# Performance work log

Hardware: AMD Instinct MI355X
Metric: run time of the kernel (lower is better)

## Reference

```python
import jax, jax.numpy as jnp
import numpy as np

N = 262144          # batch size
C = 100             # num_classes
R0, R1 = 0.95, 1.0  # recall_range
LAM = 0.5           # lambda_pauc
LS = 0.1            # label_smoothing
MAX_PAUC = R1 - R0


def setup_inputs() -> dict:
    key = jax.random.key(0)
    k1, k2 = jax.random.split(key)
    predictions = jax.random.normal(k1, (N, C), dtype=jnp.float32)
    targets = jax.random.randint(k2, (N,), 0, C)
    weight = jnp.ones((C,), dtype=jnp.float32)
    return {"predictions": predictions, "targets": targets, "weight": weight}


def _roc_curves(scores, labels):
    """Vectorized per-class ROC. scores, labels: [C, N].
    Replaces the O(N^2) per-threshold loop with sort + cumsum (tie-correct:
    tp at threshold s_j counts ALL samples with score >= s_j)."""
    order = jnp.argsort(-scores, axis=1)                      # descending
    ss = jnp.take_along_axis(scores, order, axis=1)           # [C, N]
    sl = jnp.take_along_axis(labels, order, axis=1)           # [C, N]
    cpos = jnp.cumsum(sl, axis=1)                             # cumulative positives
    # last index within each tie-group of equal scores
    neg = -ss  # ascending
    idx = jax.vmap(lambda a: jnp.searchsorted(a, a, side='right'))(neg) - 1
    tp = jnp.take_along_axis(cpos, idx, axis=1)
    cnt = (idx + 1).astype(scores.dtype)
    fp = cnt - tp
    P = cpos[:, -1:]                       # total positives per class
    Nn = scores.shape[1] - P               # total negatives per class
    tpr = jnp.where(P > 0, tp / jnp.maximum(P, 1.0), 0.0)
    fpr = jnp.where(Nn > 0, fp / jnp.maximum(Nn, 1.0), 0.0)
    return fpr, tpr


def reference(predictions, targets, weight):
    probs = jax.nn.softmax(predictions, axis=1)               # [N, C]
    onehot = jnp.eye(C, dtype=predictions.dtype)[targets]     # [N, C]
    onehot_s = (1.0 - LS) * onehot + LS / C

    # per-class binary labels (smoothed true-class value > 0.5)
    labels = (onehot_s > 0.5).astype(predictions.dtype).T     # [C, N]
    scores = probs.T                                          # [C, N]

    fpr, tpr = _roc_curves(scores, labels)
    mask = (tpr >= R0) & (tpr <= R1)
    y = jnp.maximum(tpr - R0, 0.0)
    # tpr is monotone non-decreasing, so the recall mask is contiguous and
    # trapz over the masked subset == sum over adjacent pairs both in mask.
    pm = (mask[:, :-1] & mask[:, 1:]).astype(predictions.dtype)
    pauc = jnp.sum(0.5 * (y[:, :-1] + y[:, 1:]) * (fpr[:, 1:] - fpr[:, :-1]) * pm, axis=1)  # [C]

    avg_p_auc = jnp.sum(pauc * weight) / (jnp.sum(weight) * MAX_PAUC)
    # torch computes TP/FP via .item(): the pAUC path carries no gradient
    avg_p_auc = jax.lax.stop_gradient(jnp.clip(avg_p_auc, 0.0, 1.0))

    log_probs = jax.nn.log_softmax(predictions, axis=1)
    ce_loss = -jnp.mean(jnp.sum(onehot_s * log_probs * weight, axis=1))
    pauc_loss = 1.0 - avg_p_auc ** 2
    return (1.0 - LAM) * ce_loss + LAM * pauc_loss
```

## Files before the change

kernel.cpp:

```cpp
#include <hip/hip_runtime.h>
#include <math.h>

#define WAVE 64
constexpr int   CC      = 100;
constexpr int   MAXM    = 160;
constexpr int   BUCKET  = 4096;
constexpr int   USTRIDE = 161;
constexpr int   LCAP    = 4096;
constexpr float LSMOOTH = 0.1f;
constexpr int   TILE    = 64;
constexpr int   K3AGRID = 1024;
constexpr int   K3BGRID = 512;

__global__ __launch_bounds__(256) void k1_tile(
    const float* __restrict__ pred, const int* __restrict__ targets,
    const float* __restrict__ weight, float* __restrict__ L_out,
    float* __restrict__ pos_out, float* __restrict__ ce_partial, int N)
{
    __shared__ float tile[TILE * CC];
    __shared__ int   ttgt[TILE];
    __shared__ float tL[TILE], tpos[TILE];
    __shared__ float cered[4];
    const int tid = threadIdx.x;
    const int r0  = blockIdx.x * TILE;

    const float4* src = (const float4*)(pred + (size_t)r0 * CC);
    #pragma unroll
    for (int t = tid; t < TILE * (CC / 4); t += 256)
        *((float4*)&tile[t * 4]) = src[t];
    if (tid < TILE) ttgt[tid] = targets[r0 + tid];
    __syncthreads();

    const int x = tid & 15;
    const int G = tid >> 4;
    float w[7];
    #pragma unroll
    for (int j = 0; j < 7; ++j) {
        int c = x + 16 * j;
        w[j] = (c < CC) ? weight[c] : 0.0f;
    }
    float Wl = 0.0f;
    #pragma unroll
    for (int j = 0; j < 7; ++j) Wl += w[j];
    #pragma unroll
    for (int off = 1; off < 16; off <<= 1) Wl += __shfl_xor(Wl, off, 16);

    float ce_acc = 0.0f;
    #pragma unroll
    for (int rr = 0; rr < 4; ++rr) {
        const int r = G * 4 + rr;
        const float* rp = tile + r * CC;
        float v[7];
        #pragma unroll
        for (int j = 0; j < 7; ++j) {
            int c = x + 16 * j;
            v[j] = (c < CC) ? rp[c] : -INFINITY;
        }
        float vmax = v[0];
        #pragma unroll
        for (int j = 1; j < 7; ++j) vmax = fmaxf(vmax, v[j]);
        #pragma unroll
        for (int off = 1; off < 16; off <<= 1) vmax = fmaxf(vmax, __shfl_xor(vmax, off, 16));
        float z = 0.0f, ws = 0.0f;
        #pragma unroll
        for (int j = 0; j < 7; ++j) {
            int c = x + 16 * j;
            if (c < CC) { z += __expf(v[j] - vmax); ws += w[j] * v[j]; }
        }
        #pragma unroll
        for (int off = 1; off < 16; off <<= 1) {
            z  += __shfl_xor(z,  off, 16);
            ws += __shfl_xor(ws, off, 16);
        }
        float L = vmax + __logf(z);
        if (x == 0) {
            int t = ttgt[r];
            float pt = rp[t];
            tL[r] = L; tpos[r] = pt - L;
            ce_acc += -((1.0f - LSMOOTH) * weight[t] * (pt - L)
                        + (LSMOOTH / CC) * (ws - Wl * L));
        }
    }
    #pragma unroll
    for (int off = 32; off; off >>= 1) ce_acc += __shfl_xor(ce_acc, off, WAVE);
    if ((tid & 63) == 0) cered[tid >> 6] = ce_acc;
    __syncthreads();
    if (tid < TILE) {
        L_out[r0 + tid]   = tL[tid];
        pos_out[r0 + tid] = tpos[tid];
    }
    if (tid == 0)
        ce_partial[blockIdx.x] = cered[0] + cered[1] + cered[2] + cered[3];
}

__global__ __launch_bounds__(256) void k1b_scatter(
    const int* __restrict__ targets, const float* __restrict__ pos,
    int* __restrict__ cls_cnt, float* __restrict__ bucket, int N)
{
    __shared__ int hist[CC];
    __shared__ int base[CC];
    __shared__ int loc[CC];
    const int tid = threadIdx.x;
    const int rowsPerBlock = N / gridDim.x;
    const int r0 = blockIdx.x * rowsPerBlock;
    const int r1 = r0 + rowsPerBlock;
    for (int c = tid; c < CC; c += blockDim.x) { hist[c] = 0; loc[c] = 0; }
    __syncthreads();
    for (int r = r0 + tid; r < r1; r += blockDim.x)
        atomicAdd(&hist[targets[r]], 1);
    __syncthreads();
    for (int c = tid; c < CC; c += blockDim.x)
        base[c] = (hist[c] > 0) ? atomicAdd(&cls_cnt[c], hist[c]) : 0;
    __syncthreads();
    for (int r = r0 + tid; r < r1; r += blockDim.x) {
        int c = targets[r];
        int idx = base[c] + atomicAdd(&loc[c], 1);
        if (idx < BUCKET) bucket[(size_t)c * BUCKET + idx] = pos[r];
    }
}

__global__ __launch_bounds__(256) void k2_select(
    const float* __restrict__ bucket, const int* __restrict__ cls_cnt,
    float* __restrict__ u, int* __restrict__ m_arr, int* __restrict__ P_arr,
    float* __restrict__ wm_arr)
{
    __shared__ unsigned int keys[BUCKET];
    __shared__ unsigned int hist[256];
    __shared__ unsigned int scan[256];
    __shared__ unsigned int sel[256];
    __shared__ unsigned int s_prefix;
    __shared__ int s_rank;
    __shared__ int cnt_lt;
    const int c   = blockIdx.x;
    const int tid = threadIdx.x;
    const int P = min(cls_cnt[c], BUCKET);
    double Kd = 0.95 * (double)P;
    int kf = (int)floor(Kd);
    int m = P - kf;
    if (m > MAXM) m = MAXM;
    if (m < 0) m = 0;
    if (tid == 0) {
        m_arr[c] = m; P_arr[c] = P;
        wm_arr[c] = (float)((double)(kf + 1) - Kd);
        s_prefix = 0; s_rank = m - 1; cnt_lt = 0;
    }
    for (int i = tid; i < P; i += 256) {
        unsigned int b = __float_as_uint(bucket[(size_t)c * BUCKET + i]);
        keys[i] = (b & 0x80000000u) ? ~b : (b | 0x80000000u);
    }
    __syncthreads();
    if (m == 0) return;

    for (int shift = 24; shift >= 0; shift -= 8) {
        hist[tid] = 0;
        __syncthreads();
        unsigned int pref = s_prefix;
        for (int i = tid; i < P; i += 256) {
            unsigned int k = keys[i];
            bool match = (shift == 24) || ((k >> (shift + 8)) == pref);
            if (match) atomicAdd(&hist[(k >> shift) & 255u], 1u);
        }
        __syncthreads();
        if (tid < 64) {
            unsigned h0 = hist[tid*4], h1 = hist[tid*4+1],
                     h2 = hist[tid*4+2], h3 = hist[tid*4+3];
            unsigned s0 = h0, s1 = s0 + h1, s2 = s1 + h2, s3 = s2 + h3;
            unsigned sc = s3;
            #pragma unroll
            for (int off = 1; off < 64; off <<= 1) {
                unsigned t2 = __shfl_up(sc, (unsigned)off, 64);
                if (tid >= off) sc += t2;
            }
            unsigned excl = sc - s3;
            scan[tid*4]   = excl + s0;
            scan[tid*4+1] = excl + s1;
            scan[tid*4+2] = excl + s2;
            scan[tid*4+3] = excl + s3;
        }
        __syncthreads();
        int r = s_rank;
        unsigned int inc = scan[tid];
        unsigned int exc = inc - hist[tid];
        __syncthreads();
        if ((unsigned int)r >= exc && (unsigned int)r < inc) {
            s_rank   = r - (int)exc;
            s_prefix = (pref << 8) | (unsigned int)tid;
        }
        __syncthreads();
    }
    const unsigned int kth = s_prefix;

    for (int i = tid; i < P; i += 256) {
        unsigned int k = keys[i];
        if (k < kth) {
            int pslot = atomicAdd(&cnt_lt, 1);
            sel[pslot] = k;
        }
    }
    __syncthreads();
    const int nlt = cnt_lt;
    for (int j = nlt + tid; j < 256; j += 256) sel[j] = (j < m) ? kth : 0xFFFFFFFFu;
    __syncthreads();
    for (int kk = 2; kk <= 256; kk <<= 1) {
        for (int j = kk >> 1; j > 0; j >>= 1) {
            int i = tid, ixj = tid ^ j;
            if (ixj > i) {
                unsigned int a = sel[i], b = sel[ixj];
                bool up = ((i & kk) == 0);
                if ((a > b) == up) { sel[i] = b; sel[ixj] = a; }
            }
            __syncthreads();
        }
    }
    if (tid < m) {
        unsigned int k = sel[tid];
        unsigned int b = (k & 0x80000000u) ? (k & 0x7fffffffu) : ~k;
        u[c * MAXM + tid] = __uint_as_float(b);
    }
}

__device__ __forceinline__ int ubound(const float* uc, int m, float key, int maxidx) {
    int l = 0;
    #pragma unroll
    for (int s = 128; s; s >>= 1) {
        int p = l + s - 1;
        float val = uc[p < maxidx ? p : maxidx];
        l += ((p < m) && (val <= key)) ? s : 0;
    }
    return l;
}

__global__ __launch_bounds__(256) void k3a_stream(
    const float4* __restrict__ pred4, const float* __restrict__ L,
    const float* __restrict__ u, const int* __restrict__ m_arr,
    uint2* __restrict__ list, int* __restrict__ list_cnt, int list_cap,
    int* __restrict__ g_cnt, int* __restrict__ g_sum, int total4)
{
    __shared__ float umax_s[CC];
    __shared__ uint2 buf[LCAP];
    __shared__ int lcnt;
    __shared__ int gbase;
    const int tid  = threadIdx.x;
    const int lane = tid & 63;
    if (tid < CC) {
        int m = m_arr[tid];
        umax_s[tid] = (m > 0) ? u[tid * MAXM + m - 1] : -INFINITY;
    }
    if (tid == 0) lcnt = 0;
    __syncthreads();

    auto pushq = [&](bool qual, int c, float sc) {
        unsigned long long mask = __ballot(qual);
        if (mask == 0ull) return;
        int lead = __ffsll((long long)mask) - 1;
        int nq   = __popcll(mask);
        int base = 0;
        if (lane == lead) base = atomicAdd(&lcnt, nq);
        base = __shfl(base, lead);
        if (qual) {
            int my  = __popcll(mask & ((1ull << lane) - 1ull));
            int idx = base + my;
            if (idx < LCAP) {
                buf[idx] = make_uint2((unsigned int)c, __float_as_uint(sc));
            } else {
                int m = m_arr[c];
                int l = ubound(u + c * MAXM, m, sc, MAXM - 1);
                atomicAdd(&g_cnt[c], 1);
                atomicAdd(&g_sum[c], m - 1 - l);
            }
        }
    };

    auto proc = [&](float4 v, float Ln, int j) {
        float4 um = *((const float4*)&umax_s[j * 4]);
        pushq(v.x - Ln < um.x, j * 4 + 0, v.x - Ln);
        pushq(v.y - Ln < um.y, j * 4 + 1, v.y - Ln);
        pushq(v.z - Ln < um.z, j * 4 + 2, v.z - Ln);
        pushq(v.w - Ln < um.w, j * 4 + 3, v.w - Ln);
    };

    const int stride = K3AGRID * 256;
    int i = blockIdx.x * 256 + tid;
    while (i < total4) {
        const int ia = i + stride, ib = i + 2 * stride, ic = i + 3 * stride;
        const bool ha = ia < total4, hb = ib < total4, hc = ic < total4;
        float4 v0 = pred4[i];
        float4 va = ha ? pred4[ia] : make_float4(0.f, 0.f, 0.f, 0.f);
        float4 vb = hb ? pred4[ib] : make_float4(0.f, 0.f, 0.f, 0.f);
        float4 vc = hc ? pred4[ic] : make_float4(0.f, 0.f, 0.f, 0.f);
        int n0 = i / 25, j0 = i - n0 * 25;
        float L0 = L[n0];
        proc(v0, L0, j0);
        if (ha) { int na = ia / 25, ja = ia - na * 25; proc(va, L[na], ja); }
        if (hb) { int nb = ib / 25, jb = ib - nb * 25; proc(vb, L[nb], jb); }
        if (hc) { int nc = ic / 25, jc = ic - nc * 25; proc(vc, L[nc], jc); }
        i += 4 * stride;
    }
    __syncthreads();
    int cnt = min(lcnt, LCAP);
    if (tid == 0) gbase = atomicAdd(list_cnt, cnt);
    __syncthreads();
    const int base0 = gbase;
    for (int k = tid; k < cnt; k += 256) {
        int gi = base0 + k;
        if (gi < list_cap) {
            list[gi] = buf[k];
        } else {
            uint2 e = buf[k];
            int c = (int)e.x; float sc = __uint_as_float(e.y);
            int m = m_arr[c];
            int l = ubound(u + c * MAXM, m, sc, MAXM - 1);
            atomicAdd(&g_cnt[c], 1);
            atomicAdd(&g_sum[c], m - 1 - l);
        }
    }
}

__global__ __launch_bounds__(256) void k3b_rank_final(
    const uint2* __restrict__ list, const int* __restrict__ list_cnt, int list_cap,
    const float* __restrict__ u, const int* __restrict__ m_arr,
    const int* __restrict__ P_arr, const float* __restrict__ wm_arr,
    const float* __restrict__ weight, const float* __restrict__ ce_partial,
    int nPartial, int* __restrict__ g_cnt, int* __restrict__ g_sum,
    int* __restrict__ done, float* __restrict__ out, int N)
{
    __shared__ float us[CC * USTRIDE];
    __shared__ int sm[CC], lcnt[CC], lsum[CC];
    __shared__ int lastflag;
    __shared__ double r1[256], r2[256], r3[256];
    const int tid = threadIdx.x;
    for (int c = tid; c < CC; c += 256) { sm[c] = m_arr[c]; lcnt[c] = 0; lsum[c] = 0; }
    for (int t = tid; t < CC * MAXM; t += 256) {
        int c = t / MAXM, k = t - c * MAXM;
        us[c * USTRIDE + k] = u[t];
    }
    __syncthreads();
    const int n = min(*list_cnt, list_cap);
    const int stride = K3BGRID * 256;
    for (int base = blockIdx.x * 256 + tid; base < n; base += 4 * stride) {
        int  cc4[4]; int mm4[4]; float kk4[4]; bool hh4[4];
        #pragma unroll
        for (int t = 0; t < 4; ++t) {
            int idx = base + t * stride;
            bool h = idx < n;
            uint2 e = h ? list[idx] : make_uint2(0u, 0u);
            hh4[t] = h;
            cc4[t] = (int)e.x;
            mm4[t] = h ? sm[(int)e.x] : 0;
            kk4[t] = __uint_as_float(e.y);
        }
        int ll4[4] = {0, 0, 0, 0};
        #pragma unroll
        for (int s = 128; s; s >>= 1) {
            #pragma unroll
            for (int t = 0; t < 4; ++t) {
                int p = ll4[t] + s - 1;
                float val = us[cc4[t] * USTRIDE + (p < USTRIDE - 1 ? p : USTRIDE - 1)];
                ll4[t] += ((p < mm4[t]) && (val <= kk4[t])) ? s : 0;
            }
        }
        #pragma unroll
        for (int t = 0; t < 4; ++t)
            if (hh4[t]) {
                atomicAdd(&lcnt[cc4[t]], 1);
                atomicAdd(&lsum[cc4[t]], mm4[t] - 1 - ll4[t]);
            }
    }
    __syncthreads();
    for (int c = tid; c < CC; c += 256)
        if (lcnt[c]) { atomicAdd(&g_cnt[c], lcnt[c]); atomicAdd(&g_sum[c], lsum[c]); }
    __threadfence();
    __syncthreads();
    if (tid == 0) {
        int r = atomicAdd(done, 1);
        lastflag = (r == (int)gridDim.x - 1) ? 1 : 0;
    }
    __syncthreads();
    if (!lastflag) return;

    double ce = 0.0;
    for (int t = tid; t < nPartial; t += 256) ce += (double)ce_partial[t];
    double p = 0.0, wsum = 0.0;
    for (int c = tid; c < CC; c += 256) {
        int P = P_arr[c], m = m_arr[c];
        double wgt = (double)weight[c];
        long long Nn = (long long)N - P;
        if (P > 0 && Nn > 0 && m > 0) {
            int gc = __hip_atomic_load(&g_cnt[c], __ATOMIC_RELAXED, __HIP_MEMORY_SCOPE_AGENT);
            int gs = __hip_atomic_load(&g_sum[c], __ATOMIC_RELAXED, __HIP_MEMORY_SCOPE_AGENT);
            double wm = (double)wm_arr[c];
            double S   = (double)gs + wm * (double)gc;
            double sub = 0.5 * (double)(m - 1) * (double)(m - 2) + wm * (double)(m - 1);
            double pc  = (S - sub) / ((double)Nn * (double)P);
            if (pc < 0.0) pc = 0.0;
            p += pc * wgt;
        }
        wsum += wgt;
    }
    r1[tid] = ce; r2[tid] = p; r3[tid] = wsum;
    __syncthreads();
    for (int off = 128; off; off >>= 1) {
        if (tid < off) {
            r1[tid] += r1[tid + off];
            r2[tid] += r2[tid + off];
            r3[tid] += r3[tid + off];
        }
        __syncthreads();
    }
    if (tid == 0) {
        double ce_loss = r1[0] / (double)N;
        double avg = r2[0] / (r3[0] * 0.05);
        avg = fmin(fmax(avg, 0.0), 1.0);
        out[0] = (float)(0.5 * ce_loss + 0.5 * (1.0 - avg * avg));
    }
}

extern "C" void kernel_launch(void* const* d_in, const int* in_sizes, int n_in,
                              void* d_out, int out_size, void* d_ws, size_t ws_size,
                              hipStream_t stream) {
    (void)n_in; (void)out_size;
    const float* pred    = (const float*)d_in[0];
    const int*   targets = (const int*)d_in[1];
    const float* weight  = (const float*)d_in[2];
    float* out = (float*)d_out;
    const int N = in_sizes[1];

    const int K1_BLOCKS = N / TILE;
    char* base = (char*)d_ws;
    size_t off = 0;
    auto take = [&](size_t bytes) { char* q = base + off; off += (bytes + 15) & ~(size_t)15; return q; };
    float* L_ws       = (float*)take((size_t)N * 4);
    float* pos_ws     = (float*)take((size_t)N * 4);
    float* ce_partial = (float*)take((size_t)K1_BLOCKS * 4);
    float* u          = (float*)take((size_t)CC * MAXM * 4);
    int*   m_arr      = (int*)take(CC * 4);
    int*   P_arr      = (int*)take(CC * 4);
    float* wm_arr     = (float*)take(CC * 4);
    int*   zero_blk   = (int*)take(304 * 4);
    int*   cls_cnt  = zero_blk;
    int*   g_cnt    = zero_blk + CC;
    int*   g_sum    = zero_blk + 2 * CC;
    int*   list_cnt = zero_blk + 3 * CC;
    int*   done     = zero_blk + 3 * CC + 1;
    float* bucket     = (float*)take((size_t)CC * BUCKET * 4);
    uint2* list       = (uint2*)(base + off);
    long long rem     = (long long)ws_size - (long long)off;
    int list_cap      = (rem > 0) ? (int)(rem / 8) : 0;

    hipMemsetAsync(zero_blk, 0, 304 * 4, stream);

    k1_tile<<<K1_BLOCKS, 256, 0, stream>>>(pred, targets, weight, L_ws, pos_ws,
                                           ce_partial, N);
    k1b_scatter<<<256, 256, 0, stream>>>(targets, pos_ws, cls_cnt, bucket, N);
    k2_select<<<CC, 256, 0, stream>>>(bucket, cls_cnt, u, m_arr, P_arr, wm_arr);
    const int total4 = (int)((size_t)N * CC / 4);
    k3a_stream<<<K3AGRID, 256, 0, stream>>>((const float4*)pred, L_ws, u, m_arr,
                                            list, list_cnt, list_cap, g_cnt, g_sum, total4);
    k3b_rank_final<<<K3BGRID, 256, 0, stream>>>(list, list_cnt, list_cap, u, m_arr,
                                                P_arr, wm_arr, weight, ce_partial,
                                                K1_BLOCKS, g_cnt, g_sum, done, out, N);
}
```

Measured before the change: 281.4 us.

## Fuse class scatter into k1 and simplify k3a qualifier push

Merges the per-class bucket scatter into the row-tile kernel: each block builds a shared histogram of its targets, reserves per-class slots with global atomics, and writes the positive log-prob scores straight into the buckets. This removes the pos workspace buffer and one kernel launch along with its reads of targets and pos. Separately, k3a replaces the wave-aggregated ballot push with a per-lane shared atomic and cuts the streaming unroll from 4 to 2 loads in flight. More shared-memory atomic contention and less memory-level parallelism may offset the gains, and bucket order changes but selection is order-independent.

```diff
diff --git a/kernel.cpp b/kernel.cpp
--- a/kernel.cpp
+++ b/kernel.cpp
@@ -15,12 +15,14 @@
 __global__ __launch_bounds__(256) void k1_tile(
     const float* __restrict__ pred, const int* __restrict__ targets,
     const float* __restrict__ weight, float* __restrict__ L_out,
-    float* __restrict__ pos_out, float* __restrict__ ce_partial, int N)
+    float* __restrict__ ce_partial, int* __restrict__ cls_cnt,
+    float* __restrict__ bucket, int N)
 {
     __shared__ float tile[TILE * CC];
     __shared__ int   ttgt[TILE];
     __shared__ float tL[TILE], tpos[TILE];
     __shared__ float cered[4];
+    __shared__ int   hist[CC], loc[CC], basec[CC];
     const int tid = threadIdx.x;
     const int r0  = blockIdx.x * TILE;
 
@@ -29,6 +31,7 @@
     for (int t = tid; t < TILE * (CC / 4); t += 256)
         *((float4*)&tile[t * 4]) = src[t];
     if (tid < TILE) ttgt[tid] = targets[r0 + tid];
+    for (int c = tid; c < CC; c += 256) { hist[c] = 0; loc[c] = 0; }
     __syncthreads();
 
     const int x = tid & 15;
@@ -77,6 +80,7 @@
             int t = ttgt[r];
             float pt = rp[t];
             tL[r] = L; tpos[r] = pt - L;
+            atomicAdd(&hist[t], 1);
             ce_acc += -((1.0f - LSMOOTH) * weight[t] * (pt - L)
                         + (LSMOOTH / CC) * (ws - Wl * L));
         }
@@ -85,37 +89,18 @@
     for (int off = 32; off; off >>= 1) ce_acc += __shfl_xor(ce_acc, off, WAVE);
     if ((tid & 63) == 0) cered[tid >> 6] = ce_acc;
     __syncthreads();
-    if (tid < TILE) {
-        L_out[r0 + tid]   = tL[tid];
-        pos_out[r0 + tid] = tpos[tid];
-    }
+
+    for (int c = tid; c < CC; c += 256)
+        basec[c] = hist[c] ? atomicAdd(&cls_cnt[c], hist[c]) : 0;
+    if (tid < TILE) L_out[r0 + tid] = tL[tid];
     if (tid == 0)
         ce_partial[blockIdx.x] = cered[0] + cered[1] + cered[2] + cered[3];
-}
-
-__global__ __launch_bounds__(256) void k1b_scatter(
-    const int* __restrict__ targets, const float* __restrict__ pos,
-    int* __restrict__ cls_cnt, float* __restrict__ bucket, int N)
-{
-    __shared__ int hist[CC];
-    __shared__ int base[CC];
-    __shared__ int loc[CC];
-    const int tid = threadIdx.x;
-    const int rowsPerBlock = N / gridDim.x;
-    const int r0 = blockIdx.x * rowsPerBlock;
-    const int r1 = r0 + rowsPerBlock;
-    for (int c = tid; c < CC; c += blockDim.x) { hist[c] = 0; loc[c] = 0; }
-    __syncthreads();
-    for (int r = r0 + tid; r < r1; r += blockDim.x)
-        atomicAdd(&hist[targets[r]], 1);
-    __syncthreads();
-    for (int c = tid; c < CC; c += blockDim.x)
-        base[c] = (hist[c] > 0) ? atomicAdd(&cls_cnt[c], hist[c]) : 0;
-    __syncthreads();
-    for (int r = r0 + tid; r < r1; r += blockDim.x) {
-        int c = targets[r];
-        int idx = base[c] + atomicAdd(&loc[c], 1);
-        if (idx < BUCKET) bucket[(size_t)c * BUCKET + idx] = pos[r];
+    __syncthreads();
+
+    if (tid < TILE) {
+        int c = ttgt[tid];
+        int idx = basec[c] + atomicAdd(&loc[c], 1);
+        if (idx < BUCKET) bucket[(size_t)c * BUCKET + idx] = tpos[tid];
     }
 }
 
@@ -240,8 +225,7 @@
     __shared__ uint2 buf[LCAP];
     __shared__ int lcnt;
     __shared__ int gbase;
-    const int tid  = threadIdx.x;
-    const int lane = tid & 63;
+    const int tid = threadIdx.x;
     if (tid < CC) {
         int m = m_arr[tid];
         umax_s[tid] = (m > 0) ? u[tid * MAXM + m - 1] : -INFINITY;
@@ -249,52 +233,43 @@
     if (tid == 0) lcnt = 0;
     __syncthreads();
 
-    auto pushq = [&](bool qual, int c, float sc) {
-        unsigned long long mask = __ballot(qual);
-        if (mask == 0ull) return;
-        int lead = __ffsll((long long)mask) - 1;
-        int nq   = __popcll(mask);
-        int base = 0;
-        if (lane == lead) base = atomicAdd(&lcnt, nq);
-        base = __shfl(base, lead);
-        if (qual) {
-            int my  = __popcll(mask & ((1ull << lane) - 1ull));
-            int idx = base + my;
-            if (idx < LCAP) {
-                buf[idx] = make_uint2((unsigned int)c, __float_as_uint(sc));
-            } else {
-                int m = m_arr[c];
-                int l = ubound(u + c * MAXM, m, sc, MAXM - 1);
-                atomicAdd(&g_cnt[c], 1);
-                atomicAdd(&g_sum[c], m - 1 - l);
-            }
-        }
-    };
-
     auto proc = [&](float4 v, float Ln, int j) {
         float4 um = *((const float4*)&umax_s[j * 4]);
-        pushq(v.x - Ln < um.x, j * 4 + 0, v.x - Ln);
-        pushq(v.y - Ln < um.y, j * 4 + 1, v.y - Ln);
-        pushq(v.z - Ln < um.z, j * 4 + 2, v.z - Ln);
-        pushq(v.w - Ln < um.w, j * 4 + 3, v.w - Ln);
+        float s0 = v.x - Ln, s1 = v.y - Ln, s2 = v.z - Ln, s3 = v.w - Ln;
+        #pragma unroll
+        for (int q = 0; q < 4; ++q) {
+            float scv = (q == 0) ? s0 : (q == 1) ? s1 : (q == 2) ? s2 : s3;
+            float mx  = (q == 0) ? um.x : (q == 1) ? um.y : (q == 2) ? um.z : um.w;
+            if (scv < mx) {
+                int c = j * 4 + q;
+                int idx = atomicAdd(&lcnt, 1);
+                if (idx < LCAP) {
+                    buf[idx] = make_uint2((unsigned int)c, __float_as_uint(scv));
+                } else {
+                    int m = m_arr[c];
+                    int l = ubound(u + c * MAXM, m, scv, MAXM - 1);
+                    atomicAdd(&g_cnt[c], 1);
+                    atomicAdd(&g_sum[c], m - 1 - l);
+                }
+            }
+        }
     };
 
     const int stride = K3AGRID * 256;
     int i = blockIdx.x * 256 + tid;
     while (i < total4) {
-        const int ia = i + stride, ib = i + 2 * stride, ic = i + 3 * stride;
-        const bool ha = ia < total4, hb = ib < total4, hc = ic < total4;
+        int i2 = i + stride;
+        bool has2 = (i2 < total4);
         float4 v0 = pred4[i];
-        float4 va = ha ? pred4[ia] : make_float4(0.f, 0.f, 0.f, 0.f);
-        float4 vb = hb ? pred4[ib] : make_float4(0.f, 0.f, 0.f, 0.f);
-        float4 vc = hc ? pred4[ic] : make_float4(0.f, 0.f, 0.f, 0.f);
+        float4 v1 = has2 ? pred4[i2] : make_float4(0.f, 0.f, 0.f, 0.f);
         int n0 = i / 25, j0 = i - n0 * 25;
         float L0 = L[n0];
         proc(v0, L0, j0);
-        if (ha) { int na = ia / 25, ja = ia - na * 25; proc(va, L[na], ja); }
-        if (hb) { int nb = ib / 25, jb = ib - nb * 25; proc(vb, L[nb], jb); }
-        if (hc) { int nc = ic / 25, jc = ic - nc * 25; proc(vc, L[nc], jc); }
-        i += 4 * stride;
+        if (has2) {
+            int n1 = i2 / 25, j1 = i2 - n1 * 25;
+            proc(v1, L[n1], j1);
+        }
+        i += 2 * stride;
     }
     __syncthreads();
     int cnt = min(lcnt, LCAP);
@@ -307,9 +282,9 @@
             list[gi] = buf[k];
         } else {
             uint2 e = buf[k];
-            int c = (int)e.x; float sc = __uint_as_float(e.y);
+            int c = (int)e.x; float scv = __uint_as_float(e.y);
             int m = m_arr[c];
-            int l = ubound(u + c * MAXM, m, sc, MAXM - 1);
+            int l = ubound(u + c * MAXM, m, scv, MAXM - 1);
             atomicAdd(&g_cnt[c], 1);
             atomicAdd(&g_sum[c], m - 1 - l);
         }
@@ -430,7 +405,6 @@
     size_t off = 0;
     auto take = [&](size_t bytes) { char* q = base + off; off += (bytes + 15) & ~(size_t)15; return q; };
     float* L_ws       = (float*)take((size_t)N * 4);
-    float* pos_ws     = (float*)take((size_t)N * 4);
     float* ce_partial = (float*)take((size_t)K1_BLOCKS * 4);
     float* u          = (float*)take((size_t)CC * MAXM * 4);
     int*   m_arr      = (int*)take(CC * 4);
@@ -449,9 +423,8 @@
 
     hipMemsetAsync(zero_blk, 0, 304 * 4, stream);
 
-    k1_tile<<<K1_BLOCKS, 256, 0, stream>>>(pred, targets, weight, L_ws, pos_ws,
-                                           ce_partial, N);
-    k1b_scatter<<<256, 256, 0, stream>>>(targets, pos_ws, cls_cnt, bucket, N);
+    k1_tile<<<K1_BLOCKS, 256, 0, stream>>>(pred, targets, weight, L_ws,
+                                           ce_partial, cls_cnt, bucket, N);
     k2_select<<<CC, 256, 0, stream>>>(bucket, cls_cnt, u, m_arr, P_arr, wm_arr);
     const int total4 = (int)((size_t)N * CC / 4);
     k3a_stream<<<K3AGRID, 256, 0, stream>>>((const float4*)pred, L_ws, u, m_arr,
```

Result: slower. 345.3 us (+22.7%).
